# Performance work log

Hardware: AMD Instinct MI355X
Metric: run time of the kernel (lower is better)

Reference implementation:

```python
import jax, jax.numpy as jnp
import numpy as np

S, HID, H, KH, D = 2048, 3584, 28, 4, 128
G = H // KH  # GQA group size = 7
EPS = 1e-6
THETA = 1000000.0


def _rmsnorm(x, w, eps=EPS):
    v = jnp.mean(x.astype(jnp.float32) ** 2, axis=-1, keepdims=True)
    return (x * jax.lax.rsqrt(v + eps)).astype(x.dtype) * w


def setup_inputs() -> dict:
    key = jax.random.key(0)
    k1, k2, k3, k4 = jax.random.split(key, 4)
    return {
        "positions": jnp.arange(S, dtype=jnp.int32),
        "hidden_states": jax.random.normal(k1, (S, HID), dtype=jnp.float32),
        "qkv_w": jax.random.normal(k2, ((H + 2 * KH) * D, HID), dtype=jnp.float32) * (1.0 / np.sqrt(HID)),
        "qkv_b": jax.random.normal(k3, ((H + 2 * KH) * D,), dtype=jnp.float32) * 0.02,
        "q_norm_w": jnp.ones((H * D,), dtype=jnp.float32),
        "k_norm_w": jnp.ones((KH * D,), dtype=jnp.float32),
        "o_w": jax.random.normal(k4, (HID, H * D), dtype=jnp.float32) * (1.0 / np.sqrt(H * D)),
    }


def reference(positions, hidden_states, qkv_w, qkv_b, q_norm_w, k_norm_w, o_w):
    # QKV projection (fused linear, bias=True)
    qkv = hidden_states @ qkv_w.T + qkv_b  # [S, (H+2*KH)*D]
    q, k, v = jnp.split(qkv, [H * D, H * D + KH * D], axis=-1)

    # olmo-style QK RMSNorm over the full (all-heads-concatenated) q/k vectors
    q = _rmsnorm(q, q_norm_w)
    k = _rmsnorm(k, k_norm_w)

    # NeoX-style RoPE (vLLM default): rotate halves
    half = D // 2
    inv_freq = 1.0 / (THETA ** (jnp.arange(0, D, 2, dtype=jnp.float32) / D))  # [D/2]
    freqs = positions[:, None].astype(jnp.float32) * inv_freq  # [S, D/2]
    cos = jnp.cos(freqs)[:, None, :]  # [S, 1, D/2]
    sin = jnp.sin(freqs)[:, None, :]

    def rope(x, nh):
        x = x.reshape(S, nh, D)
        x1, x2 = x[..., :half], x[..., half:]
        return jnp.concatenate([x1 * cos - x2 * sin, x2 * cos + x1 * sin], axis=-1)

    q = rope(q, H)            # [S, H, D]
    k = rope(k, KH)           # [S, KH, D]
    v = v.reshape(S, KH, D)   # [S, KH, D]

    # Grouped-query causal attention
    qg = q.reshape(S, KH, G, D)
    scores = jnp.einsum('skgd,tkd->kgst', qg, k) * (D ** -0.5)  # [KH, G, S, S]
    causal = positions[:, None] >= positions[None, :]  # [S, S]
    scores = jnp.where(causal[None, None], scores, jnp.finfo(scores.dtype).min)
    probs = jax.nn.softmax(scores, axis=-1)
    attn = jnp.einsum('kgst,tkd->skgd', probs, v).reshape(S, H * D)

    # Output projection (bias=False)
    return attn @ o_w.T  # [S, HID]
```

## Files before the change

### kernel.cpp

```cpp
#include <hip/hip_runtime.h>
#include <hip/hip_bf16.h>
#include <stdint.h>

#define S_LEN 2048
#define HIDDEN 3584
#define NH 28
#define NKH 4
#define DH 128
#define NG 7
#define NQKV 4608
#define QD 3584
#define KD 512

using bf16x8 = __attribute__((ext_vector_type(8))) __bf16;
using f32x4  = __attribute__((ext_vector_type(4))) float;
using f32x16 = __attribute__((ext_vector_type(16))) float;
using uint2v = __attribute__((ext_vector_type(2))) unsigned;

#define AS3(p) ((__attribute__((address_space(3))) void*)(p))
#define AS1(p) ((const __attribute__((address_space(1))) void*)(p))

__device__ __forceinline__ unsigned short f2bf(float f) {
    unsigned u = __float_as_uint(f);
    u += 0x7FFFu + ((u >> 16) & 1u);
    return (unsigned short)(u >> 16);
}
__device__ __forceinline__ unsigned cvtpk(float a, float b) {
    unsigned r;
    asm("v_cvt_pk_bf16_f32 %0, %1, %2" : "=v"(r) : "v"(a), "v"(b));
    return r;
}
__device__ __forceinline__ float bflo(unsigned u)  { return __uint_as_float(u << 16); }
__device__ __forceinline__ float bfhi(unsigned u)  { return __uint_as_float(u & 0xffff0000u); }
__device__ __forceinline__ float bf1(unsigned short us) { return __uint_as_float((unsigned)us << 16); }

__global__ void cvt2_f32_bf16(const float* __restrict__ a, unsigned short* __restrict__ oa, int na4,
                              const float* __restrict__ b, unsigned short* __restrict__ ob, int nb4) {
    int i = blockIdx.x * blockDim.x + threadIdx.x;
    const float* src;
    unsigned short* dst;
    int n;
    if (i < na4)            { src = a; dst = oa; n = i; }
    else if (i < na4 + nb4) { src = b; dst = ob; n = i - na4; }
    else return;
    float4 v = ((const float4*)src)[n];
    ushort4 o;
    o.x = f2bf(v.x); o.y = f2bf(v.y); o.z = f2bf(v.z); o.w = f2bf(v.w);
    ((ushort4*)dst)[n] = o;
}

template<int BN, bool BF16OUT>
__global__ __launch_bounds__(512, 2) void gemm_deep(
    const unsigned short* __restrict__ A,
    const unsigned short* __restrict__ B,
    void* __restrict__ Cv,
    const float* __restrict__ bias,
    int M, int N, int K)
{
    constexpr int NF    = BN / 32;
    constexpr int HNF   = NF / 2;
    constexpr int WN    = BN / 2;
    constexpr int VB    = BN / 64;
    constexpr int TILEB = (256 + BN) * 128;
    __shared__ __align__(16) unsigned char ds[2 * TILEB];

    const int tid  = threadIdx.x;
    const int w    = tid >> 6;
    const int lane = tid & 63;
    const int lr   = lane & 15;
    const int lg   = lane >> 4;
    const int wr   = w >> 1;
    const int wc   = w & 1;
    const int m0   = blockIdx.y * 256;
    const int n0   = blockIdx.x * BN;
    const long K2  = (long)K * 2;
    const int scw  = 16 * ((tid & 7) ^ ((tid >> 3) & 7));
    const int srow = tid >> 3;
    const unsigned char* Ab = (const unsigned char*)A;
    const unsigned char* Bb = (const unsigned char*)B;
    const int nk = K >> 6;

    unsigned char* buf0 = ds;
    unsigned char* buf1 = ds + TILEB;

    auto stageB = [&](int kt, unsigned char* bufp) {
        const long kb = (long)kt * 128;
        #pragma unroll
        for (int k = 0; k < VB; ++k)
            __builtin_amdgcn_global_load_lds(
                AS1(Bb + (long)(n0 + k * 64 + srow) * K2 + kb + scw),
                AS3(bufp + k * 8192 + w * 1024), 16, 0, 0);
    };
    auto stageA = [&](int kt, unsigned char* bufp) {
        const long kb = (long)kt * 128;
        #pragma unroll
        for (int k = 0; k < 4; ++k)
            __builtin_amdgcn_global_load_lds(
                AS1(Ab + (long)(m0 + k * 64 + srow) * K2 + kb + scw),
                AS3(bufp + VB * 8192 + k * 8192 + w * 1024), 16, 0, 0);
    };

    f32x4  acc[4][NF] = {};
    bf16x8 af[4][2], bf[NF][2];

    auto readA = [&](const unsigned char* bufp) {
        #pragma unroll
        for (int i = 0; i < 4; ++i) {
            const int row = wr * 64 + i * 16 + lr;
            #pragma unroll
            for (int kk = 0; kk < 2; ++kk)
                af[i][kk] = *(const bf16x8*)(bufp + VB * 8192 + row * 128 +
                                             ((kk * 64 + lg * 16) ^ ((lr & 7) << 4)));
        }
    };
    auto readB = [&](const unsigned char* bufp) {
        #pragma unroll
        for (int ni = 0; ni < NF; ++ni) {
            const int row = wc * WN + ni * 16 + lr;
            #pragma unroll
            for (int kk = 0; kk < 2; ++kk)
                bf[ni][kk] = *(const bf16x8*)(bufp + row * 128 +
                                              ((kk * 64 + lg * 16) ^ ((lr & 7) << 4)));
        }
    };
    auto mfmah = [&](int half) {
        __builtin_amdgcn_s_setprio(1);
        #pragma unroll
        for (int i = 0; i < 4; ++i)
            #pragma unroll
            for (int n2 = 0; n2 < HNF; ++n2) {
                const int ni = half * HNF + n2;
                #pragma unroll
                for (int kk = 0; kk < 2; ++kk)
                    acc[i][ni] = __builtin_amdgcn_mfma_f32_16x16x32_bf16(
                        af[i][kk], bf[ni][kk], acc[i][ni], 0, 0, 0);
            }
        __builtin_amdgcn_s_setprio(0);
    };

    #define VMC() do { if constexpr (VB == 3) asm volatile("s_waitcnt vmcnt(3)" ::: "memory"); \
                       else                   asm volatile("s_waitcnt vmcnt(2)" ::: "memory"); } while (0)
    #define LGK0() do { asm volatile("s_waitcnt lgkmcnt(0)" ::: "memory"); \
                        __builtin_amdgcn_sched_barrier(0); } while (0)

    stageB(0, buf0); stageA(0, buf0); stageB(1, buf1);
    VMC();
    __builtin_amdgcn_s_barrier();

    const int npairs = nk >> 1;
    for (int p = 0; p < npairs; ++p) {
        const int to = 2 * p + 1;
        int te2 = 2 * p + 2; if (te2 >= nk) te2 = nk - 1;
        int to2 = 2 * p + 3; if (to2 >= nk) to2 = nk - 1;

        readA(buf0); readB(buf0);
        stageA(to, buf1);
        __builtin_amdgcn_s_barrier();
        LGK0();
        mfmah(0);
        __builtin_amdgcn_s_barrier();
        stageB(te2, buf0);
        mfmah(1);
        VMC();
        __builtin_amdgcn_s_barrier();

        readA(buf1); readB(buf1);
        stageA(te2, buf0);
        __builtin_amdgcn_s_barrier();
        LGK0();
        mfmah(0);
        __builtin_amdgcn_s_barrier();
        stageB(to2, buf1);
        mfmah(1);
        VMC();
        __builtin_amdgcn_s_barrier();
    }
    asm volatile("s_waitcnt vmcnt(0)" ::: "memory");

    #pragma unroll
    for (int mi = 0; mi < 4; ++mi) {
        #pragma unroll
        for (int ni = 0; ni < NF; ++ni) {
            const int col = n0 + wc * WN + ni * 16 + lr;
            const float bv = bias ? bias[col] : 0.0f;
            #pragma unroll
            for (int j = 0; j < 4; ++j) {
                const int row = m0 + wr * 64 + mi * 16 + lg * 4 + j;
                if constexpr (BF16OUT)
                    ((unsigned short*)Cv)[(long)row * N + col] = f2bf(acc[mi][ni][j] + bv);
                else
                    ((float*)Cv)[(long)row * N + col] = acc[mi][ni][j] + bv;
            }
        }
    }
    #undef VMC
    #undef LGK0
}

__global__ __launch_bounds__(256) void qkv_post(
    const unsigned short* __restrict__ qkv,
    const int* __restrict__ positions,
    const float* __restrict__ qnw,
    const float* __restrict__ knw,
    unsigned short* __restrict__ qb,
    unsigned short* __restrict__ kb,
    unsigned short* __restrict__ vt2)
{
    const int s   = blockIdx.x;
    const int tid = threadIdx.x;
    const unsigned short* rowp = qkv + (long)s * NQKV;
    __shared__ float red[256];
    __shared__ float s_rq, s_rk;

    float aq = 0.f;
    for (int i = tid; i < QD / 8; i += 256) {
        const unsigned* u2 = (const unsigned*)(rowp + i * 8);
        #pragma unroll
        for (int j = 0; j < 4; ++j) {
            const float lo = bflo(u2[j]), hi = bfhi(u2[j]);
            aq += lo * lo + hi * hi;
        }
    }
    red[tid] = aq; __syncthreads();
    for (int off = 128; off > 0; off >>= 1) {
        if (tid < off) red[tid] += red[tid + off];
        __syncthreads();
    }
    if (tid == 0) s_rq = rsqrtf(red[0] / (float)QD + 1e-6f);
    __syncthreads();

    float ak = 0.f;
    if (tid < KD / 8) {
        const unsigned* u2 = (const unsigned*)(rowp + QD + tid * 8);
        #pragma unroll
        for (int j = 0; j < 4; ++j) {
            const float lo = bflo(u2[j]), hi = bfhi(u2[j]);
            ak += lo * lo + hi * hi;
        }
    }
    red[tid] = ak; __syncthreads();
    for (int off = 128; off > 0; off >>= 1) {
        if (tid < off) red[tid] += red[tid + off];
        __syncthreads();
    }
    if (tid == 0) s_rk = rsqrtf(red[0] / (float)KD + 1e-6f);
    __syncthreads();

    const float rq  = s_rq, rk = s_rk * 0.08838834764831845f;
    const float pos = (float)positions[s];
    const float c_lnf = 0.21586735253866598f;

    for (int u = tid; u < NH * 64; u += 256) {
        const int h = u >> 6, j = u & 63;
        const float inv = expf(-(float)j * c_lnf);
        float sn, cs;
        sincosf(pos * inv, &sn, &cs);
        const float x1 = bf1(rowp[h * DH + j])      * rq * qnw[h * DH + j];
        const float x2 = bf1(rowp[h * DH + 64 + j]) * rq * qnw[h * DH + 64 + j];
        qb[((long)h * S_LEN + s) * DH + j]      = f2bf(x1 * cs - x2 * sn);
        qb[((long)h * S_LEN + s) * DH + 64 + j] = f2bf(x2 * cs + x1 * sn);
    }
    for (int u = tid; u < NKH * 64; u += 256) {
        const int h = u >> 6, j = u & 63;
        const float inv = expf(-(float)j * c_lnf);
        float sn, cs;
        sincosf(pos * inv, &sn, &cs);
        const float x1 = bf1(rowp[QD + h * DH + j])      * rk * knw[h * DH + j];
        const float x2 = bf1(rowp[QD + h * DH + 64 + j]) * rk * knw[h * DH + 64 + j];
        kb[((long)h * S_LEN + s) * DH + j]      = f2bf(x1 * cs - x2 * sn);
        kb[((long)h * S_LEN + s) * DH + 64 + j] = f2bf(x2 * cs + x1 * sn);
    }
    for (int u = tid; u < KD; u += 256) {
        const int hh = u >> 7, d = u & 127;
        vt2[(((long)hh * (S_LEN / 32) + (s >> 5)) * DH + d) * 32 + (s & 31)] =
            rowp[QD + KD + u];
    }
}

__global__ __launch_bounds__(512) void attn_fwd(
    const unsigned short* __restrict__ qb,
    const unsigned short* __restrict__ kb,
    const unsigned short* __restrict__ vt2,
    unsigned short* __restrict__ attnb,
    const float* __restrict__ ow,
    unsigned short* __restrict__ w2)
{
    const int tid  = threadIdx.x;

    if (blockIdx.x >= 64) {
        const int ci = (blockIdx.x - 64) * NKH + blockIdx.y;
        const int n4 = HIDDEN * QD / 4;
        for (int i = ci * 512 + tid; i < n4; i += 64 * 512) {
            float4 v = ((const float4*)ow)[i];
            ushort4 o;
            o.x = f2bf(v.x); o.y = f2bf(v.y); o.z = f2bf(v.z); o.w = f2bf(v.w);
            ((ushort4*)w2)[i] = o;
        }
        return;
    }

    __shared__ __align__(16) unsigned char sK[2][8192];
    __shared__ __align__(16) unsigned char sV[2][8192];

    const int qt   = 63 - blockIdx.x;
    const int kh   = blockIdx.y;
    const int w    = tid >> 6;
    const int lane = tid & 63;
    const int lq   = lane & 31;
    const int hi   = lane >> 5;
    const int hi8  = hi * 8;
    const int hi4  = hi * 4;
    const int q0   = qt * 32;
    const int NT   = qt + 1;

    const unsigned char* kgb = (const unsigned char*)(kb + (long)kh * S_LEN * DH);
    const unsigned char* vgb = (const unsigned char*)vt2 + (long)kh * (S_LEN / 32) * 8192;

    const int ksrc_off = (((tid & 15) ^ (tid >> 4)) & 15) << 4;
    const int u        = tid & 255;
    const int vsrc_off = ((u & 3) ^ ((u >> 3) & 3)) << 4;

    const float RTHR = 8.0f;

    bf16x8 qf[8];
    if (w < 7) {
        const int h = kh * NG + w;
        const unsigned short* qrow = qb + ((long)h * S_LEN + q0 + lq) * DH;
        #pragma unroll
        for (int c = 0; c < 8; ++c)
            qf[c] = *(const bf16x8*)(qrow + c * 16 + hi8);
    }

    f32x16 o[4] = {};
    float m = -3e38f;
    float l = 0.f;

    if (tid < 256) {
        #pragma unroll
        for (int j = 0; j < 2; ++j)
            __builtin_amdgcn_global_load_lds(AS1(kgb + ((tid >> 4) + 16 * j) * 256 + ksrc_off),
                                             AS3(&sK[0][0] + w * 1024 + j * 4096), 16, 0, 0);
    } else {
        #pragma unroll
        for (int j = 0; j < 2; ++j)
            __builtin_amdgcn_global_load_lds(AS1(vgb + ((u >> 2) + 64 * j) * 64 + vsrc_off),
                                             AS3(&sV[0][0] + (w - 4) * 1024 + j * 4096), 16, 0, 0);
    }

    for (int t = 0; t < NT; ++t) {
        __syncthreads();

        if (t + 1 < NT) {
            const int b = (t + 1) & 1;
            if (tid < 256) {
                const unsigned char* ks = kgb + (long)(t + 1) * 8192;
                #pragma unroll
                for (int j = 0; j < 2; ++j)
                    __builtin_amdgcn_global_load_lds(AS1(ks + ((tid >> 4) + 16 * j) * 256 + ksrc_off),
                                                     AS3(&sK[b][0] + w * 1024 + j * 4096), 16, 0, 0);
            } else {
                const unsigned char* vs = vgb + (long)(t + 1) * 8192;
                #pragma unroll
                for (int j = 0; j < 2; ++j)
                    __builtin_amdgcn_global_load_lds(AS1(vs + ((u >> 2) + 64 * j) * 64 + vsrc_off),
                                                     AS3(&sV[b][0] + (w - 4) * 1024 + j * 4096), 16, 0, 0);
            }
        }

        if (w < 7) {
            const unsigned char* sKb = sK[t & 1];
            const unsigned char* sVb = sV[t & 1];

            bf16x8 kf[8];
            #pragma unroll
            for (int c = 0; c < 8; ++c)
                kf[c] = *(const bf16x8*)(sKb + lq * 256 + (((2 * c + hi) ^ (lq & 15)) << 4));
            f32x16 sc = {};
            __builtin_amdgcn_s_setprio(1);
            #pragma unroll
            for (int c = 0; c < 8; ++c)
                sc = __builtin_amdgcn_mfma_f32_32x32x16_bf16(kf[c], qf[c], sc, 0, 0, 0);
            __builtin_amdgcn_s_setprio(0);

            float s[16];
            if (t == NT - 1) {
                #pragma unroll
                for (int r = 0; r < 16; ++r) {
                    const int kr = (r & 3) + 8 * (r >> 2) + hi4;
                    s[r] = (kr > lq) ? -3e38f : sc[r];
                }
            } else {
                #pragma unroll
                for (int r = 0; r < 16; ++r) s[r] = sc[r];
            }

            float mx = s[0];
            #pragma unroll
            for (int r = 1; r < 16; ++r) mx = fmaxf(mx, s[r]);
            mx = fmaxf(mx, __shfl_xor(mx, 32));

            if (!__all(mx <= m + RTHR)) {
                const float nm  = fmaxf(m, mx);
                const float fac = __expf(m - nm);
                l *= fac;
                #pragma unroll
                for (int d0 = 0; d0 < 4; ++d0)
                    #pragma unroll
                    for (int r = 0; r < 16; ++r) o[d0][r] *= fac;
                m = nm;
            }

            float p[16];
            float ps = 0.f;
            #pragma unroll
            for (int r = 0; r < 16; ++r) {
                p[r] = __expf(s[r] - m);
                ps += p[r];
            }
            ps += __shfl_xor(ps, 32);
            l += ps;

            unsigned pa01 = cvtpk(p[0],  p[1]),  pa23 = cvtpk(p[2],  p[3]);
            unsigned pb01 = cvtpk(p[4],  p[5]),  pb23 = cvtpk(p[6],  p[7]);
            unsigned pc01 = cvtpk(p[8],  p[9]),  pc23 = cvtpk(p[10], p[11]);
            unsigned pd01 = cvtpk(p[12], p[13]), pd23 = cvtpk(p[14], p[15]);
            uint2v r0 = __builtin_amdgcn_permlane32_swap(pa01, pb01, false, false);
            uint2v r1 = __builtin_amdgcn_permlane32_swap(pa23, pb23, false, false);
            uint2v r2 = __builtin_amdgcn_permlane32_swap(pc01, pd01, false, false);
            uint2v r3 = __builtin_amdgcn_permlane32_swap(pc23, pd23, false, false);

            union { unsigned uu[4]; bf16x8 v; } pf0, pf1;
            pf0.uu[0] = r0[0];
            pf0.uu[1] = r1[0];
            pf0.uu[2] = r0[1];
            pf0.uu[3] = r1[1];
            pf1.uu[0] = r2[0];
            pf1.uu[1] = r3[0];
            pf1.uu[2] = r2[1];
            pf1.uu[3] = r3[1];

            #pragma unroll
            for (int d0 = 0; d0 < 4; ++d0) {
                const int row = d0 * 32 + lq;
                const int sw  = (lq >> 1) & 3;
                bf16x8 vf0 = *(const bf16x8*)(sVb + row * 64 + ((hi ^ sw) << 4));
                bf16x8 vf1 = *(const bf16x8*)(sVb + row * 64 + (((2 + hi) ^ sw) << 4));
                __builtin_amdgcn_s_setprio(1);
                o[d0] = __builtin_amdgcn_mfma_f32_32x32x16_bf16(vf0, pf0.v, o[d0], 0, 0, 0);
                o[d0] = __builtin_amdgcn_mfma_f32_32x32x16_bf16(vf1, pf1.v, o[d0], 0, 0, 0);
                __builtin_amdgcn_s_setprio(0);
            }
        }
    }

    if (w == 7) return;

    const float rl = 1.0f / l;
    unsigned short* orow = attnb + (long)(q0 + lq) * QD + (kh * NG + w) * DH;
    #pragma unroll
    for (int d0 = 0; d0 < 4; ++d0) {
        #pragma unroll
        for (int g = 0; g < 4; ++g) {
            ushort4 s4;
            s4.x = f2bf(o[d0][4 * g + 0] * rl);
            s4.y = f2bf(o[d0][4 * g + 1] * rl);
            s4.z = f2bf(o[d0][4 * g + 2] * rl);
            s4.w = f2bf(o[d0][4 * g + 3] * rl);
            *(ushort4*)(orow + d0 * 32 + 8 * g + hi4) = s4;
        }
    }
}

extern "C" void kernel_launch(void* const* d_in, const int* in_sizes, int n_in,
                              void* d_out, int out_size, void* d_ws, size_t ws_size,
                              hipStream_t stream) {
    const int*   positions = (const int*)d_in[0];
    const float* hidden    = (const float*)d_in[1];
    const float* qkv_w     = (const float*)d_in[2];
    const float* qkv_b     = (const float*)d_in[3];
    const float* qnw       = (const float*)d_in[4];
    const float* knw       = (const float*)d_in[5];
    const float* o_w       = (const float*)d_in[6];
    float* out = (float*)d_out;

    unsigned char* ws = (unsigned char*)d_ws;
    unsigned short* hb    = (unsigned short*)(ws);
    unsigned short* w1    = (unsigned short*)(ws + 14680064);
    unsigned short* qkvb  = (unsigned short*)(ws + 47710208);
    unsigned short* qbuf  = (unsigned short*)(ws + 85458944);
    unsigned short* kbuf  = (unsigned short*)(ws + 100139008);
    unsigned short* vtb   = (unsigned short*)(ws + 102236160);
    unsigned short* attnb = (unsigned short*)(ws);
    unsigned short* w2    = (unsigned short*)(ws + 14680064);

    const int na4 = S_LEN * HIDDEN / 4;
    const int nb4 = NQKV * HIDDEN / 4;
    cvt2_f32_bf16<<<(na4 + nb4 + 255) / 256, 256, 0, stream>>>(hidden, hb, na4, qkv_w, w1, nb4);
    gemm_deep<192, true><<<dim3(NQKV / 192, S_LEN / 256), 512, 0, stream>>>(
        hb, w1, qkvb, qkv_b, S_LEN, NQKV, HIDDEN);
    qkv_post<<<S_LEN, 256, 0, stream>>>(qkvb, positions, qnw, knw, qbuf, kbuf, vtb);
    attn_fwd<<<dim3(64 + 16, NKH), 512, 0, stream>>>(qbuf, kbuf, vtb, attnb, o_w, w2);
    gemm_deep<128, false><<<dim3(HIDDEN / 128, S_LEN / 256), 512, 0, stream>>>(
        attnb, w2, out, nullptr, S_LEN, HIDDEN, QD);
}
```

Before: 240.9 us.

## Split causal attention KV loop into two interleaved halves plus combine kernel

The attention kernel now runs a third grid dimension of two splits. Each split processes alternate KV tiles and writes unnormalized bf16 partial outputs plus per-row max and sum. A new combine kernel merges the two partials with rescaled softmax statistics and writes the normalized attention output. The goal is to double the number of attention blocks and spread the causal triangle's uneven work across more CUs. The cost is an extra kernel launch, partial-output write and read traffic, and bf16 rounding of the unnormalized partials.

```diff
diff --git a/kernel.cpp b/kernel.cpp
--- a/kernel.cpp
+++ b/kernel.cpp
@@ -277,20 +277,22 @@
     }
 }
 
-__global__ __launch_bounds__(512) void attn_fwd(
+__global__ __launch_bounds__(512) void attn_split(
     const unsigned short* __restrict__ qb,
     const unsigned short* __restrict__ kb,
     const unsigned short* __restrict__ vt2,
-    unsigned short* __restrict__ attnb,
+    unsigned short* __restrict__ pOb,
+    float* __restrict__ pml,
     const float* __restrict__ ow,
     unsigned short* __restrict__ w2)
 {
-    const int tid  = threadIdx.x;
+    const int tid = threadIdx.x;
 
     if (blockIdx.x >= 64) {
+        if (blockIdx.z != 0) return;
         const int ci = (blockIdx.x - 64) * NKH + blockIdx.y;
         const int n4 = HIDDEN * QD / 4;
-        for (int i = ci * 512 + tid; i < n4; i += 64 * 512) {
+        for (int i = ci * 512 + tid; i < n4; i += 128 * 512) {
             float4 v = ((const float4*)ow)[i];
             ushort4 o;
             o.x = f2bf(v.x); o.y = f2bf(v.y); o.z = f2bf(v.z); o.w = f2bf(v.w);
@@ -304,6 +306,7 @@
 
     const int qt   = 63 - blockIdx.x;
     const int kh   = blockIdx.y;
+    const int z    = blockIdx.z;
     const int w    = tid >> 6;
     const int lane = tid & 63;
     const int lq   = lane & 31;
@@ -322,6 +325,22 @@
 
     const float RTHR = 8.0f;
 
+    auto stage = [&](int t, int b) {
+        if (tid < 256) {
+            const unsigned char* ks = kgb + (long)t * 8192;
+            #pragma unroll
+            for (int j = 0; j < 2; ++j)
+                __builtin_amdgcn_global_load_lds(AS1(ks + ((tid >> 4) + 16 * j) * 256 + ksrc_off),
+                                                 AS3(&sK[b][0] + w * 1024 + j * 4096), 16, 0, 0);
+        } else {
+            const unsigned char* vs = vgb + (long)t * 8192;
+            #pragma unroll
+            for (int j = 0; j < 2; ++j)
+                __builtin_amdgcn_global_load_lds(AS1(vs + ((u >> 2) + 64 * j) * 64 + vsrc_off),
+                                                 AS3(&sV[b][0] + (w - 4) * 1024 + j * 4096), 16, 0, 0);
+        }
+    };
+
     bf16x8 qf[8];
     if (w < 7) {
         const int h = kh * NG + w;
@@ -335,41 +354,17 @@
     float m = -3e38f;
     float l = 0.f;
 
-    if (tid < 256) {
-        #pragma unroll
-        for (int j = 0; j < 2; ++j)
-            __builtin_amdgcn_global_load_lds(AS1(kgb + ((tid >> 4) + 16 * j) * 256 + ksrc_off),
-                                             AS3(&sK[0][0] + w * 1024 + j * 4096), 16, 0, 0);
-    } else {
-        #pragma unroll
-        for (int j = 0; j < 2; ++j)
-            __builtin_amdgcn_global_load_lds(AS1(vgb + ((u >> 2) + 64 * j) * 64 + vsrc_off),
-                                             AS3(&sV[0][0] + (w - 4) * 1024 + j * 4096), 16, 0, 0);
-    }
-
-    for (int t = 0; t < NT; ++t) {
+    stage(z, 0);
+
+    int ii = 0;
+    for (int t = z; t < NT; t += 2, ++ii) {
         __syncthreads();
 
-        if (t + 1 < NT) {
-            const int b = (t + 1) & 1;
-            if (tid < 256) {
-                const unsigned char* ks = kgb + (long)(t + 1) * 8192;
-                #pragma unroll
-                for (int j = 0; j < 2; ++j)
-                    __builtin_amdgcn_global_load_lds(AS1(ks + ((tid >> 4) + 16 * j) * 256 + ksrc_off),
-                                                     AS3(&sK[b][0] + w * 1024 + j * 4096), 16, 0, 0);
-            } else {
-                const unsigned char* vs = vgb + (long)(t + 1) * 8192;
-                #pragma unroll
-                for (int j = 0; j < 2; ++j)
-                    __builtin_amdgcn_global_load_lds(AS1(vs + ((u >> 2) + 64 * j) * 64 + vsrc_off),
-                                                     AS3(&sV[b][0] + (w - 4) * 1024 + j * 4096), 16, 0, 0);
-            }
-        }
+        if (t + 2 < NT) stage(t + 2, (ii + 1) & 1);
 
         if (w < 7) {
-            const unsigned char* sKb = sK[t & 1];
-            const unsigned char* sVb = sV[t & 1];
+            const unsigned char* sKb = sK[ii & 1];
+            const unsigned char* sVb = sV[ii & 1];
 
             bf16x8 kf[8];
             #pragma unroll
@@ -455,19 +450,64 @@
 
     if (w == 7) return;
 
-    const float rl = 1.0f / l;
-    unsigned short* orow = attnb + (long)(q0 + lq) * QD + (kh * NG + w) * DH;
+    const long rec = ((long)(z * NKH + kh) * 64 + qt) * 7 + w;
+    unsigned short* Orec = pOb + rec * 4096;
     #pragma unroll
     for (int d0 = 0; d0 < 4; ++d0) {
         #pragma unroll
         for (int g = 0; g < 4; ++g) {
-            ushort4 s4;
-            s4.x = f2bf(o[d0][4 * g + 0] * rl);
-            s4.y = f2bf(o[d0][4 * g + 1] * rl);
-            s4.z = f2bf(o[d0][4 * g + 2] * rl);
-            s4.w = f2bf(o[d0][4 * g + 3] * rl);
-            *(ushort4*)(orow + d0 * 32 + 8 * g + hi4) = s4;
-        }
+            uint2v pk;
+            pk[0] = cvtpk(o[d0][4 * g + 0], o[d0][4 * g + 1]);
+            pk[1] = cvtpk(o[d0][4 * g + 2], o[d0][4 * g + 3]);
+            *(uint2v*)(Orec + lq * 128 + d0 * 32 + 8 * g + hi4) = pk;
+        }
+    }
+    if (hi == 0) {
+        pml[rec * 64 + lq]      = m;
+        pml[rec * 64 + 32 + lq] = l;
+    }
+}
+
+__global__ __launch_bounds__(256) void attn_combine(
+    const unsigned short* __restrict__ pOb,
+    const float* __restrict__ pml,
+    unsigned short* __restrict__ attnb)
+{
+    const int qt  = blockIdx.x;
+    const int h   = blockIdx.y;
+    const int kh  = h / NG;
+    const int wh  = h % NG;
+    const int tid = threadIdx.x;
+    const int q   = tid >> 3;
+    const int dg  = (tid & 7) * 16;
+
+    const long rec0 = ((long)kh * 64 + qt) * 7 + wh;
+    const long rec1 = rec0 + (long)NKH * 64 * 7;
+    const float m0 = pml[rec0 * 64 + q], l0 = pml[rec0 * 64 + 32 + q];
+    const float m1 = pml[rec1 * 64 + q], l1 = pml[rec1 * 64 + 32 + q];
+    const float M  = fmaxf(m0, m1);
+    const float f0 = __expf(m0 - M);
+    const float f1 = __expf(m1 - M);
+    const float rl = 1.0f / (l0 * f0 + l1 * f1);
+
+    const unsigned short* O0 = pOb + rec0 * 4096 + q * 128 + dg;
+    const unsigned short* O1 = pOb + rec1 * 4096 + q * 128 + dg;
+    unsigned short* orow = attnb + (long)(qt * 32 + q) * QD + h * DH + dg;
+    #pragma unroll
+    for (int i = 0; i < 2; ++i) {
+        uint4 a = *(const uint4*)(O0 + i * 8);
+        uint4 b = *(const uint4*)(O1 + i * 8);
+        ushort4 s0, s1;
+        s0.x = f2bf((f0 * bflo(a.x) + f1 * bflo(b.x)) * rl);
+        s0.y = f2bf((f0 * bfhi(a.x) + f1 * bfhi(b.x)) * rl);
+        s0.z = f2bf((f0 * bflo(a.y) + f1 * bflo(b.y)) * rl);
+        s0.w = f2bf((f0 * bfhi(a.y) + f1 * bfhi(b.y)) * rl);
+        s1.x = f2bf((f0 * bflo(a.z) + f1 * bflo(b.z)) * rl);
+        s1.y = f2bf((f0 * bfhi(a.z) + f1 * bfhi(b.z)) * rl);
+        s1.z = f2bf((f0 * bflo(a.w) + f1 * bflo(b.w)) * rl);
+        s1.w = f2bf((f0 * bfhi(a.w) + f1 * bfhi(b.w)) * rl);
+        *(ushort4*)(orow + i * 8)     = s0;
+        *(ushort4*)(orow + i * 8 + 4) = s1;
     }
 }
 
@@ -492,6 +532,8 @@
     unsigned short* vtb   = (unsigned short*)(ws + 102236160);
     unsigned short* attnb = (unsigned short*)(ws);
     unsigned short* w2    = (unsigned short*)(ws + 14680064);
+    unsigned short* pOb   = (unsigned short*)(ws + 47710208);
+    float*          pml   = (float*)(ws + 77070336);
 
     const int na4 = S_LEN * HIDDEN / 4;
     const int nb4 = NQKV * HIDDEN / 4;
@@ -499,7 +541,8 @@
     gemm_deep<192, true><<<dim3(NQKV / 192, S_LEN / 256), 512, 0, stream>>>(
         hb, w1, qkvb, qkv_b, S_LEN, NQKV, HIDDEN);
     qkv_post<<<S_LEN, 256, 0, stream>>>(qkvb, positions, qnw, knw, qbuf, kbuf, vtb);
-    attn_fwd<<<dim3(64 + 16, NKH), 512, 0, stream>>>(qbuf, kbuf, vtb, attnb, o_w, w2);
+    attn_split<<<dim3(64 + 32, NKH, 2), 512, 0, stream>>>(qbuf, kbuf, vtb, pOb, pml, o_w, w2);
+    attn_combine<<<dim3(S_LEN / 32, NH), 256, 0, stream>>>(pOb, pml, attnb);
     gemm_deep<128, false><<<dim3(HIDDEN / 128, S_LEN / 256), 512, 0, stream>>>(
         attnb, w2, out, nullptr, S_LEN, HIDDEN, QD);
 }
```

Result: slower. 252.2 us (+4.7%).
